# Kernel optimization log

Measured on AMD Instinct MI355X. Metric: run time of the kernel, lower is better.

The kernel has to match this reference:

```python
import jax, jax.numpy as jnp
import numpy as np

IM_MAX = 1.0
IM_SIZE = 128
N_THRESHOLDS = 64


def _thresholds():
    # end = im_size * sqrt(2) // 2  (float32 math, floor-div) -> 90.0
    end = np.float32(np.float32(IM_SIZE) * np.sqrt(np.float32(2.0))) // np.float32(2.0)
    t = np.linspace(2.0, float(end), N_THRESHOLDS, dtype=np.float32)
    return np.round(t).astype(np.int32)  # half-to-even, matches torch.round


def _masks():
    # stack of circular low-pass masks, one per threshold: [T, H, W]
    crow, ccol = IM_SIZE // 2, IM_SIZE // 2
    y = np.arange(IM_SIZE)[:, None]
    x = np.arange(IM_SIZE)[None, :]
    r2 = (x - ccol) ** 2 + (y - crow) ** 2  # [H, W]
    thr = _thresholds().astype(np.int64)
    m = (r2[None, :, :] <= (thr[:, None, None] ** 2)).astype(np.float32)
    return jnp.asarray(m)


def setup_inputs() -> dict:
    key = jax.random.key(0)
    k1, k2 = jax.random.split(key)
    shape = (256, 3, IM_SIZE, IM_SIZE)
    prediction = jax.random.uniform(k1, shape, dtype=jnp.float32)
    gt = jax.random.uniform(k2, shape, dtype=jnp.float32)
    return {"prediction": prediction, "gt": gt}


def reference(prediction, gt):
    # Single FFT pass on each input (original redundantly recomputes per threshold,
    # but mask is 0/1 so masked-diff energy = mask * |pred_f - gt_f|^2).
    pf = jnp.fft.fftshift(jnp.fft.fft2(prediction), axes=(-2, -1))  # [B,C,H,W] c64
    gf = jnp.fft.fftshift(jnp.fft.fft2(gt), axes=(-2, -1))
    diff = pf - gf
    sq_err = diff.real ** 2 + diff.imag ** 2  # |.|^2, [B,C,H,W] f32
    masks = _masks()  # [T,H,W]
    # sum_sq_error per (batch, threshold): sum over C,H,W with mask
    sum_sq = jnp.einsum('thw,bchw->bt', masks, sq_err)  # [B,T]
    n_pixels = IM_SIZE * IM_SIZE
    const = 20.0 * jnp.log10(jnp.float32(IM_MAX * n_pixels))
    cf_psnr = const - 10.0 * jnp.log10(sum_sq)
    return cf_psnr
```

## Files before the change

### kernel.cpp

```cpp
#include <hip/hip_runtime.h>
#include <hip/hip_fp16.h>

#define IMG 128
#define NPIX (IMG * IMG)
#define NT 64
#define LSU 129
#define ZN (64 * LSU)

__device__ __constant__ int c_thr[NT] = {
    2, 3, 5, 6, 8, 9, 10, 12, 13, 15, 16, 17, 19, 20, 22, 23,
    24, 26, 27, 29, 30, 31, 33, 34, 36, 37, 38, 40, 41, 43, 44, 45,
    47, 48, 49, 51, 52, 54, 55, 56, 58, 59, 61, 62, 63, 65, 66, 68,
    69, 70, 72, 73, 75, 76, 77, 79, 80, 82, 83, 84, 86, 87, 89, 90};

__device__ __forceinline__ int rev7(int x) { return (int)(__brev((unsigned)x) >> 25); }

__device__ __forceinline__ unsigned packh2(float x, float y) {
    __half2 h = __floats2half2_rn(x, y);
    return *reinterpret_cast<unsigned*>(&h);
}
__device__ __forceinline__ float2 unpackh2(unsigned u) {
    __half2 h;
    *reinterpret_cast<unsigned*>(&h) = u;
    return __half22float2(h);
}

__device__ __forceinline__ float x1f(float v) {
    return __int_as_float(__builtin_amdgcn_mov_dpp(__float_as_int(v), 0xB1, 0xF, 0xF, true));
}
__device__ __forceinline__ float x2f(float v) {
    return __int_as_float(__builtin_amdgcn_mov_dpp(__float_as_int(v), 0x4E, 0xF, 0xF, true));
}
__device__ __forceinline__ float x3f(float v) {
    return __int_as_float(__builtin_amdgcn_mov_dpp(__float_as_int(v), 0x1B, 0xF, 0xF, true));
}
__device__ __forceinline__ float x7f(float v) {
    return __int_as_float(__builtin_amdgcn_mov_dpp(__float_as_int(v), 0x141, 0xF, 0xF, true));
}
__device__ __forceinline__ float x4f(float v) { return x7f(x3f(v)); }
__device__ __forceinline__ float x8f(float v) {
    return __int_as_float(__builtin_amdgcn_mov_dpp(__float_as_int(v), 0x128, 0xF, 0xF, true));
}


#define BFLY(ar, ai, br, bi, wc, wsn)    \
    do {                                 \
        const float dr_ = (ar) - (br);   \
        const float di_ = (ai) - (bi);   \
        (ar) += (br);                    \
        (ai) += (bi);                    \
        (br) = dr_ * (wc)-di_ * (wsn);   \
        (bi) = dr_ * (wsn) + di_ * (wc); \
    } while (0)

#define XSTAGE(vr, vi, XF, cc, ss, sg)                  \
    do {                                                \
        _Pragma("unroll") for (int j = 0; j < 8; ++j) { \
            const float pr_ = XF(vr[j]), pi_ = XF(vi[j]); \
            const float xr_ = fmaf((sg), vr[j], pr_);   \
            const float xi_ = fmaf((sg), vi[j], pi_);   \
            vr[j] = xr_ * (cc)-xi_ * (ss);              \
            vi[j] = xr_ * (ss) + xi_ * (cc);            \
        }                                               \
    } while (0)

#define FFT128(vr, vi)                                                \
    do {                                                              \
        _Pragma("unroll") for (int j = 0; j < 4; ++j)                 \
            BFLY(vr[j], vi[j], vr[j + 4], vi[j + 4], c64[j], s64[j]); \
        BFLY(vr[0], vi[0], vr[2], vi[2], c32[0], s32[0]);             \
        BFLY(vr[1], vi[1], vr[3], vi[3], c32[1], s32[1]);             \
        BFLY(vr[4], vi[4], vr[6], vi[6], c32[0], s32[0]);             \
        BFLY(vr[5], vi[5], vr[7], vi[7], c32[1], s32[1]);             \
        _Pragma("unroll") for (int j = 0; j < 8; j += 2)              \
            BFLY(vr[j], vi[j], vr[j + 1], vi[j + 1], c16v, s16v);     \
        XSTAGE(vr, vi, x8f, c8v, s8v, sg8);                           \
        XSTAGE(vr, vi, x4f, c4v, s4v, sg4);                           \
        XSTAGE(vr, vi, x2f, c2v, s2v, sg2);                           \
        _Pragma("unroll") for (int j = 0; j < 8; ++j) {               \
            const float pr_ = x1f(vr[j]), pi_ = x1f(vi[j]);           \
            vr[j] = fmaf(sg1, vr[j], pr_);                            \
            vi[j] = fmaf(sg1, vi[j], pi_);                            \
        }                                                             \
    } while (0)

#define LDROW(rr, buf)                                                 \
    do {                                                               \
        const float* pe_ = pred + base + (size_t)(2 * (rr)) * IMG;     \
        const float* ge_ = gt + base + (size_t)(2 * (rr)) * IMG;       \
        _Pragma("unroll") for (int j = 0; j < 8; ++j) {                \
            const int o_ = 16 * j + l;                                 \
            buf[j] = pe_[o_];                                          \
            buf[8 + j] = pe_[IMG + o_];                                \
            buf[16 + j] = ge_[o_];                                     \
            buf[24 + j] = ge_[IMG + o_];                               \
        }                                                              \
    } while (0)

#define STROW(rr, buf)                                            \
    do {                                                          \
        _Pragma("unroll") for (int j = 0; j < 8; ++j) {           \
            vr[j] = 0.5f * (buf[j] - buf[16 + j]);                \
            vi[j] = 0.5f * (buf[8 + j] - buf[24 + j]);            \
        }                                                         \
        FFT128(vr, vi);                                           \
        _Pragma("unroll") for (int j = 0; j < 8; ++j)             \
            s_z[(rr)*LSU + 16 * j + l] = packh2(vr[j], vi[j]);    \
    } while (0)

#define COLONE(u, wf)                                                   \
    do {                                                                \
        const int c1_ = rev7(u);                                        \
        const int c2_ = rev7((128 - (u)) & 127);                        \
        _Pragma("unroll") for (int j = 0; j < 8; ++j) {                 \
            const int rowo_ = (8 * j + zr) * LSU;                       \
            const float2 A_ = unpackh2(s_z[rowo_ + c1_]);               \
            const float2 B_ = unpackh2(s_z[rowo_ + c2_]);               \
            vr[j] = odd ? (A_.y + B_.y) : (A_.x + B_.x);                \
            vi[j] = odd ? (B_.x - A_.x) : (A_.y - B_.y);                \
        }                                                               \
        FFT128(vr, vi);                                                 \
        const float u2f_ = (float)((u) * (u));                          \
        _Pragma("unroll") for (int j = 0; j < 8; ++j) {                 \
            const float r2f_ = dy2f[j] + u2f_;                          \
            if (r2f_ <= 8100.0f) {                                      \
                const int rc_ = (int)ceilf(sqrtf(r2f_) - 3e-4f);        \
                atomicAdd(&s_h[wave][s_rc2bin[rc_]],                    \
                          (wf) * (vr[j] * vr[j] + vi[j] * vi[j]));      \
            }                                                           \
        }                                                               \
    } while (0)

__global__ void zero_out_kernel(float* __restrict__ p) {
    p[blockIdx.x * 256 + threadIdx.x] = 0.0f;
}

__global__ __launch_bounds__(512, 6) void fft_hist_kernel(const float* __restrict__ pred,
                                                          const float* __restrict__ gt,
                                                          float* __restrict__ acc) {
    __shared__ unsigned s_z[ZN];
    __shared__ float s_h[8][66];
    __shared__ int s_rc2bin[91];

    const int tid = threadIdx.x;
    const int lane = tid & 63;
    const int wave = tid >> 6;
    const int l = lane & 15;
    const int g = lane >> 4;
    const int U = wave * 4 + g;
    const int bc = blockIdx.x;
    const int b = bc / 3;

    for (int i = tid; i < 8 * 66; i += 512) (&s_h[0][0])[i] = 0.0f;
    if (tid < 91) {
        int t = 0;
        while (t < 63 && c_thr[t] < tid) ++t;
        s_rc2bin[tid] = t;
    }

    const float K = -6.2831853071795864769f * (1.0f / 128.0f);
    float c64[4], s64[4], c32[2], s32[2], c16v, s16v;
#pragma unroll
    for (int j = 0; j < 4; ++j) sincosf(K * (float)(16 * j + l), &s64[j], &c64[j]);
    sincosf(K * (float)(2 * l), &s32[0], &c32[0]);
    sincosf(K * (float)(2 * l + 32), &s32[1], &c32[1]);
    sincosf(K * (float)(4 * l), &s16v, &c16v);
    float c8v, s8v, c4v, s4v, c2v, s2v;
    sincosf(K * (float)((l & 8) ? (l & 7) * 8 : 0), &s8v, &c8v);
    sincosf(K * (float)((l & 4) ? (l & 3) * 16 : 0), &s4v, &c4v);
    sincosf(K * (float)((l & 2) ? (l & 1) * 32 : 0), &s2v, &c2v);
    const float sg8 = (l & 8) ? -1.0f : 1.0f;
    const float sg4 = (l & 4) ? -1.0f : 1.0f;
    const float sg2 = (l & 2) ? -1.0f : 1.0f;
    const float sg1 = (l & 1) ? -1.0f : 1.0f;

    const size_t base = (size_t)bc * NPIX;
    const int zr = l >> 1;
    const int odd = l & 1;

    float dy2f[8];
    const int r4 = ((l & 1) << 3) | ((l & 2) << 1) | ((l & 4) >> 1) | ((l & 8) >> 3);
#pragma unroll
    for (int j = 0; j < 8; ++j) {
        const int fy = (((j & 1) << 2) | (j & 2) | ((j & 4) >> 2)) | (r4 << 3);
        const int dy = (fy < 64) ? fy : 128 - fy;
        dy2f[j] = (float)(dy * dy);
    }

    float buf[32], vr[8], vi[8];

    LDROW(U, buf);
    STROW(U, buf);
    LDROW(U + 32, buf);
    STROW(U + 32, buf);
    __syncthreads();

    COLONE(U, (U == 0) ? 1.0f : 2.0f);
    COLONE(U + 32, 2.0f);
    if (U == 0) COLONE(64, 1.0f);
    __syncthreads();

    if (tid < 64) {
        float tot = 0.0f;
#pragma unroll
        for (int w = 0; w < 8; ++w) tot += s_h[w][tid];
        atomicAdd(&acc[b * NT + tid], tot);
    }
}

__global__ void psnr_kernel(float* __restrict__ acc) {
    __shared__ float h[NT];
    const int b = blockIdx.x, t = threadIdx.x;
    h[t] = acc[b * NT + t];
    __syncthreads();
    float cum = 0.0f;
    for (int j = 0; j <= t; ++j) cum += h[j];
    acc[b * NT + t] = 84.2883987849f - 10.0f * log10f(cum);
}

extern "C" void kernel_launch(void* const* d_in, const int* in_sizes, int n_in,
                              void* d_out, int out_size, void* d_ws, size_t ws_size,
                              hipStream_t stream) {
    const float* pred = (const float*)d_in[0];
    const float* gt = (const float*)d_in[1];
    float* out = (float*)d_out;

    zero_out_kernel<<<64, 256, 0, stream>>>(out);
    fft_hist_kernel<<<256 * 3, 512, 0, stream>>>(pred, gt, out);
    psnr_kernel<<<256, NT, 0, stream>>>(out);
}
```

Before: 61.46 us.

## Fold pred-gt subtraction into loads, issue both row loads early, use fast sin/cos

The prediction minus ground-truth difference is now formed while loading, so each row buffer holds 16 floats instead of 32. Both rows' global loads are issued before either row FFT, overlapping the second row's memory latency with the first FFT. Twiddle setup uses __sinf/__cosf intrinsics in place of full-precision sincosf. This trades some twiddle accuracy for shorter setup, and holding both row buffers at once raises register pressure.

```diff
diff --git a/kernel.cpp b/kernel.cpp
--- a/kernel.cpp
+++ b/kernel.cpp
@@ -53,15 +53,15 @@
         (bi) = dr_ * (wsn) + di_ * (wc); \
     } while (0)
 
-#define XSTAGE(vr, vi, XF, cc, ss, sg)                  \
-    do {                                                \
-        _Pragma("unroll") for (int j = 0; j < 8; ++j) { \
+#define XSTAGE(vr, vi, XF, cc, ss, sg)                    \
+    do {                                                  \
+        _Pragma("unroll") for (int j = 0; j < 8; ++j) {   \
             const float pr_ = XF(vr[j]), pi_ = XF(vi[j]); \
-            const float xr_ = fmaf((sg), vr[j], pr_);   \
-            const float xi_ = fmaf((sg), vi[j], pi_);   \
-            vr[j] = xr_ * (cc)-xi_ * (ss);              \
-            vi[j] = xr_ * (ss) + xi_ * (cc);            \
-        }                                               \
+            const float xr_ = fmaf((sg), vr[j], pr_);     \
+            const float xi_ = fmaf((sg), vi[j], pi_);     \
+            vr[j] = xr_ * (cc)-xi_ * (ss);                \
+            vi[j] = xr_ * (ss) + xi_ * (cc);              \
+        }                                                 \
     } while (0)
 
 #define FFT128(vr, vi)                                                \
@@ -84,51 +84,49 @@
         }                                                             \
     } while (0)
 
-#define LDROW(rr, buf)                                                 \
-    do {                                                               \
-        const float* pe_ = pred + base + (size_t)(2 * (rr)) * IMG;     \
-        const float* ge_ = gt + base + (size_t)(2 * (rr)) * IMG;       \
-        _Pragma("unroll") for (int j = 0; j < 8; ++j) {                \
-            const int o_ = 16 * j + l;                                 \
-            buf[j] = pe_[o_];                                          \
-            buf[8 + j] = pe_[IMG + o_];                                \
-            buf[16 + j] = ge_[o_];                                     \
-            buf[24 + j] = ge_[IMG + o_];                               \
-        }                                                              \
-    } while (0)
-
-#define STROW(rr, buf)                                            \
-    do {                                                          \
-        _Pragma("unroll") for (int j = 0; j < 8; ++j) {           \
-            vr[j] = 0.5f * (buf[j] - buf[16 + j]);                \
-            vi[j] = 0.5f * (buf[8 + j] - buf[24 + j]);            \
-        }                                                         \
-        FFT128(vr, vi);                                           \
-        _Pragma("unroll") for (int j = 0; j < 8; ++j)             \
-            s_z[(rr)*LSU + 16 * j + l] = packh2(vr[j], vi[j]);    \
-    } while (0)
-
-#define COLONE(u, wf)                                                   \
-    do {                                                                \
-        const int c1_ = rev7(u);                                        \
-        const int c2_ = rev7((128 - (u)) & 127);                        \
-        _Pragma("unroll") for (int j = 0; j < 8; ++j) {                 \
-            const int rowo_ = (8 * j + zr) * LSU;                       \
-            const float2 A_ = unpackh2(s_z[rowo_ + c1_]);               \
-            const float2 B_ = unpackh2(s_z[rowo_ + c2_]);               \
-            vr[j] = odd ? (A_.y + B_.y) : (A_.x + B_.x);                \
-            vi[j] = odd ? (B_.x - A_.x) : (A_.y - B_.y);                \
-        }                                                               \
-        FFT128(vr, vi);                                                 \
-        const float u2f_ = (float)((u) * (u));                          \
-        _Pragma("unroll") for (int j = 0; j < 8; ++j) {                 \
-            const float r2f_ = dy2f[j] + u2f_;                          \
-            if (r2f_ <= 8100.0f) {                                      \
-                const int rc_ = (int)ceilf(sqrtf(r2f_) - 3e-4f);        \
-                atomicAdd(&s_h[wave][s_rc2bin[rc_]],                    \
-                          (wf) * (vr[j] * vr[j] + vi[j] * vi[j]));      \
-            }                                                           \
-        }                                                               \
+#define LDROW(rr, buf)                                             \
+    do {                                                           \
+        const float* pe_ = pred + base + (size_t)(2 * (rr)) * IMG; \
+        const float* ge_ = gt + base + (size_t)(2 * (rr)) * IMG;   \
+        _Pragma("unroll") for (int j = 0; j < 8; ++j) {            \
+            const int o_ = 16 * j + l;                             \
+            buf[j] = 0.5f * (pe_[o_] - ge_[o_]);                   \
+            buf[8 + j] = 0.5f * (pe_[IMG + o_] - ge_[IMG + o_]);   \
+        }                                                          \
+    } while (0)
+
+#define STROW(rr, buf)                                         \
+    do {                                                       \
+        _Pragma("unroll") for (int j = 0; j < 8; ++j) {        \
+            vr[j] = buf[j];                                    \
+            vi[j] = buf[8 + j];                                \
+        }                                                      \
+        FFT128(vr, vi);                                        \
+        _Pragma("unroll") for (int j = 0; j < 8; ++j)          \
+            s_z[(rr)*LSU + 16 * j + l] = packh2(vr[j], vi[j]); \
+    } while (0)
+
+#define COLONE(u, wf)                                              \
+    do {                                                           \
+        const int c1_ = rev7(u);                                   \
+        const int c2_ = rev7((128 - (u)) & 127);                   \
+        _Pragma("unroll") for (int j = 0; j < 8; ++j) {            \
+            const int rowo_ = (8 * j + zr) * LSU;                  \
+            const float2 A_ = unpackh2(s_z[rowo_ + c1_]);          \
+            const float2 B_ = unpackh2(s_z[rowo_ + c2_]);          \
+            vr[j] = odd ? (A_.y + B_.y) : (A_.x + B_.x);           \
+            vi[j] = odd ? (B_.x - A_.x) : (A_.y - B_.y);           \
+        }                                                          \
+        FFT128(vr, vi);                                            \
+        const float u2f_ = (float)((u) * (u));                     \
+        _Pragma("unroll") for (int j = 0; j < 8; ++j) {            \
+            const float r2f_ = dy2f[j] + u2f_;                     \
+            if (r2f_ <= 8100.0f) {                                 \
+                const int rc_ = (int)ceilf(sqrtf(r2f_) - 3e-4f);   \
+                atomicAdd(&s_h[wave][s_rc2bin[rc_]],               \
+                          (wf) * (vr[j] * vr[j] + vi[j] * vi[j])); \
+            }                                                      \
+        }                                                          \
     } while (0)
 
 __global__ void zero_out_kernel(float* __restrict__ p) {
@@ -161,14 +159,27 @@
     const float K = -6.2831853071795864769f * (1.0f / 128.0f);
     float c64[4], s64[4], c32[2], s32[2], c16v, s16v;
 #pragma unroll
-    for (int j = 0; j < 4; ++j) sincosf(K * (float)(16 * j + l), &s64[j], &c64[j]);
-    sincosf(K * (float)(2 * l), &s32[0], &c32[0]);
-    sincosf(K * (float)(2 * l + 32), &s32[1], &c32[1]);
-    sincosf(K * (float)(4 * l), &s16v, &c16v);
+    for (int j = 0; j < 4; ++j) {
+        const float a = K * (float)(16 * j + l);
+        s64[j] = __sinf(a);
+        c64[j] = __cosf(a);
+    }
+    {
+        const float a0 = K * (float)(2 * l), a1 = K * (float)(2 * l + 32);
+        s32[0] = __sinf(a0); c32[0] = __cosf(a0);
+        s32[1] = __sinf(a1); c32[1] = __cosf(a1);
+        const float a2 = K * (float)(4 * l);
+        s16v = __sinf(a2); c16v = __cosf(a2);
+    }
     float c8v, s8v, c4v, s4v, c2v, s2v;
-    sincosf(K * (float)((l & 8) ? (l & 7) * 8 : 0), &s8v, &c8v);
-    sincosf(K * (float)((l & 4) ? (l & 3) * 16 : 0), &s4v, &c4v);
-    sincosf(K * (float)((l & 2) ? (l & 1) * 32 : 0), &s2v, &c2v);
+    {
+        const float a8 = K * (float)((l & 8) ? (l & 7) * 8 : 0);
+        const float a4 = K * (float)((l & 4) ? (l & 3) * 16 : 0);
+        const float a2 = K * (float)((l & 2) ? (l & 1) * 32 : 0);
+        s8v = __sinf(a8); c8v = __cosf(a8);
+        s4v = __sinf(a4); c4v = __cosf(a4);
+        s2v = __sinf(a2); c2v = __cosf(a2);
+    }
     const float sg8 = (l & 8) ? -1.0f : 1.0f;
     const float sg4 = (l & 4) ? -1.0f : 1.0f;
     const float sg2 = (l & 2) ? -1.0f : 1.0f;
@@ -187,12 +198,12 @@
         dy2f[j] = (float)(dy * dy);
     }
 
-    float buf[32], vr[8], vi[8];
-
-    LDROW(U, buf);
-    STROW(U, buf);
-    LDROW(U + 32, buf);
-    STROW(U + 32, buf);
+    float bufA[16], bufB[16], vr[8], vi[8];
+
+    LDROW(U, bufA);
+    LDROW(U + 32, bufB);
+    STROW(U, bufA);
+    STROW(U + 32, bufB);
     __syncthreads();
 
     COLONE(U, (U == 0) ? 1.0f : 2.0f);
```

Result: slower. 69.20 us (+12.6%).
